# Kernel tuning notes

Measured on AMD Instinct MI355X. Metric: run time of the kernel, lower is better.

## Reference

```python
import jax, jax.numpy as jnp
import numpy as np

B, L, D, NUM_NODES = 256, 512, 128, 1024


def setup_inputs() -> dict:
    key = jax.random.key(0)
    k1, k2, k3, k4, k5, k6 = jax.random.split(key, 6)
    src_ids = jax.random.randint(k1, (B, L), 0, NUM_NODES, dtype=jnp.int32)
    dst_ids = jax.random.randint(k2, (B, L), 0, NUM_NODES, dtype=jnp.int32)
    s = 1.0  # nn.Linear default init is uniform; randn is fine for a numeric baseline
    W1 = jax.random.normal(k3, (1, D), dtype=jnp.float32) * s
    b1 = jax.random.normal(k4, (D,), dtype=jnp.float32) * 0.01
    W2 = jax.random.normal(k5, (D, D), dtype=jnp.float32) * (1.0 / np.sqrt(D))
    b2 = jax.random.normal(k6, (D,), dtype=jnp.float32) * 0.01
    return {"src_ids": src_ids, "dst_ids": dst_ids, "W1": W1, "b1": b1, "W2": W2, "b2": b2}


def _counts_in(a, b):
    # counts_in[i, j] = number of occurrences of a[i, j] within b[i, :]
    # matches np.unique counts / dict-lookup semantics (missing key -> 0)
    return (a[:, :, None] == b[:, None, :]).sum(axis=-1).astype(jnp.float32)


def _encode(appearances, W1, b1, W2, b2):
    # appearances: (B, L, 2) -> unsqueeze(-1) -> Linear(1, D) -> ReLU -> Linear(D, D) -> sum over the 2 count channels
    h = jax.nn.relu(appearances[..., None] * W1[0] + b1)      # (B, L, 2, D)
    h = jnp.einsum('blcd,de->blce', h, W2) + b2               # (B, L, 2, D)
    return h.sum(axis=2)                                      # (B, L, D)


def reference(src_ids, dst_ids, W1, b1, W2, b2):
    # co-occurrence appearance counts
    src_app = jnp.stack([_counts_in(src_ids, src_ids), _counts_in(src_ids, dst_ids)], axis=-1)  # (B, Ls, 2)
    dst_app = jnp.stack([_counts_in(dst_ids, src_ids), _counts_in(dst_ids, dst_ids)], axis=-1)  # (B, Ld, 2)
    # zero out padded positions (node id == 0)
    src_app = jnp.where(src_ids[..., None] == 0, 0.0, src_app)
    dst_app = jnp.where(dst_ids[..., None] == 0, 0.0, dst_app)
    src_feat = _encode(src_app, W1, b1, W2, b2)
    dst_feat = _encode(dst_app, W1, b1, W2, b2)
    return src_feat, dst_feat
```

## Files before the change

### kernel.cpp

```cpp
#include <hip/hip_runtime.h>


#define BB      256
#define LL      512
#define DD      128
#define NNODES  1024
#define SPLITS  4
#define ROWS_PER (LL / SPLITS)
#define CMAXP1  (LL + 1)
#define TBL_SLOTS 64

typedef float f4x __attribute__((ext_vector_type(4)));

__global__ __launch_bounds__(256) void fused_encode_kernel(
    const int* __restrict__ src_ids, const int* __restrict__ dst_ids,
    const float* __restrict__ W1, const float* __restrict__ b1,
    const float* __restrict__ W2, const float* __restrict__ b2,
    float* __restrict__ out) {
  __shared__ __align__(16) float tbl[TBL_SLOTS * DD];
  __shared__ int slotOf[CMAXP1];
  __shared__ int cnt[4 * ROWS_PER];
  __shared__ int cOf[TBL_SLOTS];
  __shared__ int ns;

  int* hist = (int*)tbl;

  const int batch = blockIdx.x >> 2;
  const int split = blockIdx.x & (SPLITS - 1);
  const int tid   = threadIdx.x;

#pragma unroll
  for (int i = tid; i < 2 * NNODES; i += 256) hist[i] = 0;
  for (int i = tid; i < CMAXP1; i += 256) slotOf[i] = -1;
  if (tid == 0) ns = 0;
  __syncthreads();

  const int* sb = src_ids + batch * LL;
  const int* db = dst_ids + batch * LL;
#pragma unroll
  for (int i = tid; i < LL; i += 256) {
    atomicAdd(&hist[sb[i]], 1);
    atomicAdd(&hist[NNODES + db[i]], 1);
  }
  __syncthreads();

  const int r0 = split * ROWS_PER;
#pragma unroll
  for (int i = tid; i < 4 * ROWS_PER; i += 256) {
    const int r  = i & (ROWS_PER - 1);
    const int g  = i >> 7;
    const int id = (g < 2 ? sb : db)[r0 + r];
    const int c  = id ? hist[(g & 1) * NNODES + id] : 0;
    cnt[i] = c;
    slotOf[c] = 1;
  }
  __syncthreads();

  for (int c = tid; c < CMAXP1; c += 256) {
    if (slotOf[c] >= 0) {
      const int s = atomicAdd(&ns, 1);
      slotOf[c] = s;
      cOf[s] = c;
    }
  }
  __syncthreads();

#pragma unroll
  for (int i = tid; i < 4 * ROWS_PER; i += 256) cnt[i] = slotOf[cnt[i]];

  {
    const int nslots = ns;
    const int e = tid & (DD - 1);
    for (int s = tid >> 7; s < nslots; s += 2) {
      const float fc = (float)cOf[s];
      float acc = b2[e];
#pragma unroll 16
      for (int d = 0; d < DD; ++d)
        acc = fmaf(fmaxf(fmaf(fc, W1[d], b1[d]), 0.0f), W2[d * DD + e], acc);
      tbl[s * DD + e] = acc;
    }
  }
  __syncthreads();

  const int lane = tid & 31;
  const int rsub = tid >> 5;
  float* out_s = out + ((size_t)batch * LL + r0) * DD;
  float* out_d = out_s + (size_t)BB * LL * DD;
  const f4x* tb = (const f4x*)tbl;

#pragma unroll 4
  for (int rr = rsub; rr < ROWS_PER; rr += 8) {
    const f4x a = tb[cnt[rr] * (DD / 4) + lane];
    const f4x b = tb[cnt[ROWS_PER + rr] * (DD / 4) + lane];
    const f4x c = tb[cnt[2 * ROWS_PER + rr] * (DD / 4) + lane];
    const f4x d = tb[cnt[3 * ROWS_PER + rr] * (DD / 4) + lane];
    __builtin_nontemporal_store(a + b, ((f4x*)(out_s + (size_t)rr * DD)) + lane);
    __builtin_nontemporal_store(c + d, ((f4x*)(out_d + (size_t)rr * DD)) + lane);
  }
}

extern "C" void kernel_launch(void* const* d_in, const int* in_sizes, int n_in,
                              void* d_out, int out_size, void* d_ws, size_t ws_size,
                              hipStream_t stream) {
  const int*   src = (const int*)d_in[0];
  const int*   dst = (const int*)d_in[1];
  const float* W1  = (const float*)d_in[2];
  const float* b1  = (const float*)d_in[3];
  const float* W2  = (const float*)d_in[4];
  const float* b2  = (const float*)d_in[5];
  fused_encode_kernel<<<BB * SPLITS, 256, 0, stream>>>(
      src, dst, W1, b1, W2, b2, (float*)d_out);
}
```

Before: 164.0 us.

## Use one 1024-thread block per batch with packed histogram and direct-indexed count table

Replaces four 256-thread blocks per batch with a single 1024-thread block, which removes the histogram work each split block used to redo. Src and dst counts are packed into one int histogram (low and high 16 bits), and a 32-bit mask records which counts below 32 appear. Encoded rows are precomputed only for those counts and indexed directly by count value, so the slot-remapping pass goes away. Counts of 32 or more fall back to a per-lane slow path that recomputes the row. That path is correct but costly, and it will almost never run for these random inputs.

```diff
diff --git a/kernel.cpp b/kernel.cpp
--- a/kernel.cpp
+++ b/kernel.cpp
@@ -5,97 +5,99 @@
 #define LL      512
 #define DD      128
 #define NNODES  1024
-#define SPLITS  4
-#define ROWS_PER (LL / SPLITS)
-#define CMAXP1  (LL + 1)
-#define TBL_SLOTS 64
+#define TBL_C   32
 
 typedef float f4x __attribute__((ext_vector_type(4)));
 
-__global__ __launch_bounds__(256) void fused_encode_kernel(
+__device__ __noinline__ f4x slow_row(int c, int lane,
+                                     const float* __restrict__ W1,
+                                     const float* __restrict__ b1,
+                                     const float* __restrict__ W2,
+                                     const float* __restrict__ b2) {
+  const int e0 = lane * 4;
+  f4x acc = { b2[e0], b2[e0 + 1], b2[e0 + 2], b2[e0 + 3] };
+  for (int d = 0; d < DD; ++d) {
+    const float h = fmaxf(fmaf((float)c, W1[d], b1[d]), 0.0f);
+#pragma unroll
+    for (int j = 0; j < 4; ++j) acc[j] = fmaf(h, W2[d * DD + e0 + j], acc[j]);
+  }
+  return acc;
+}
+
+__global__ __launch_bounds__(1024) void fused_encode_kernel(
     const int* __restrict__ src_ids, const int* __restrict__ dst_ids,
     const float* __restrict__ W1, const float* __restrict__ b1,
     const float* __restrict__ W2, const float* __restrict__ b2,
     float* __restrict__ out) {
-  __shared__ __align__(16) float tbl[TBL_SLOTS * DD];
-  __shared__ int slotOf[CMAXP1];
-  __shared__ int cnt[4 * ROWS_PER];
-  __shared__ int cOf[TBL_SLOTS];
-  __shared__ int ns;
+  __shared__ __align__(16) float tbl[TBL_C * DD];
+  __shared__ short cnt4[LL][4];
+  __shared__ int bitc[TBL_C];
+  __shared__ int nb, mask;
 
   int* hist = (int*)tbl;
 
-  const int batch = blockIdx.x >> 2;
-  const int split = blockIdx.x & (SPLITS - 1);
+  const int batch = blockIdx.x;
   const int tid   = threadIdx.x;
 
-#pragma unroll
-  for (int i = tid; i < 2 * NNODES; i += 256) hist[i] = 0;
-  for (int i = tid; i < CMAXP1; i += 256) slotOf[i] = -1;
-  if (tid == 0) ns = 0;
+  hist[tid] = 0;
+  if (tid == 0) { nb = 0; mask = 0; }
   __syncthreads();
 
   const int* sb = src_ids + batch * LL;
   const int* db = dst_ids + batch * LL;
+  if (tid < LL) atomicAdd(&hist[sb[tid]], 1);
+  else          atomicAdd(&hist[db[tid - LL]], 0x10000);
+  __syncthreads();
+
 #pragma unroll
-  for (int i = tid; i < LL; i += 256) {
-    atomicAdd(&hist[sb[i]], 1);
-    atomicAdd(&hist[NNODES + db[i]], 1);
+  for (int i = tid; i < 4 * LL; i += 1024) {
+    const int g  = i >> 9;
+    const int r  = i & (LL - 1);
+    const int id = (g < 2 ? sb : db)[r];
+    const int hv = id ? hist[id] : 0;
+    const int c  = (g & 1) ? (hv >> 16) : (hv & 0xffff);
+    cnt4[r][g] = (short)c;
+    if (c < TBL_C) atomicOr(&mask, 1u << c);
   }
   __syncthreads();
 
-  const int r0 = split * ROWS_PER;
-#pragma unroll
-  for (int i = tid; i < 4 * ROWS_PER; i += 256) {
-    const int r  = i & (ROWS_PER - 1);
-    const int g  = i >> 7;
-    const int id = (g < 2 ? sb : db)[r0 + r];
-    const int c  = id ? hist[(g & 1) * NNODES + id] : 0;
-    cnt[i] = c;
-    slotOf[c] = 1;
+  if (tid < TBL_C && ((mask >> tid) & 1)) {
+    const int p = atomicAdd(&nb, 1);
+    bitc[p] = tid;
   }
   __syncthreads();
 
-  for (int c = tid; c < CMAXP1; c += 256) {
-    if (slotOf[c] >= 0) {
-      const int s = atomicAdd(&ns, 1);
-      slotOf[c] = s;
-      cOf[s] = c;
-    }
-  }
-  __syncthreads();
-
-#pragma unroll
-  for (int i = tid; i < 4 * ROWS_PER; i += 256) cnt[i] = slotOf[cnt[i]];
-
   {
-    const int nslots = ns;
+    const int nrows = nb;
     const int e = tid & (DD - 1);
-    for (int s = tid >> 7; s < nslots; s += 2) {
-      const float fc = (float)cOf[s];
+    for (int k = tid >> 7; k < nrows; k += 8) {
+      const int   c  = bitc[k];
+      const float fc = (float)c;
       float acc = b2[e];
 #pragma unroll 16
       for (int d = 0; d < DD; ++d)
         acc = fmaf(fmaxf(fmaf(fc, W1[d], b1[d]), 0.0f), W2[d * DD + e], acc);
-      tbl[s * DD + e] = acc;
+      tbl[c * DD + e] = acc;
     }
   }
   __syncthreads();
 
   const int lane = tid & 31;
   const int rsub = tid >> 5;
-  float* out_s = out + ((size_t)batch * LL + r0) * DD;
+  float* out_s = out + (size_t)batch * LL * DD;
   float* out_d = out_s + (size_t)BB * LL * DD;
   const f4x* tb = (const f4x*)tbl;
 
 #pragma unroll 4
-  for (int rr = rsub; rr < ROWS_PER; rr += 8) {
-    const f4x a = tb[cnt[rr] * (DD / 4) + lane];
-    const f4x b = tb[cnt[ROWS_PER + rr] * (DD / 4) + lane];
-    const f4x c = tb[cnt[2 * ROWS_PER + rr] * (DD / 4) + lane];
-    const f4x d = tb[cnt[3 * ROWS_PER + rr] * (DD / 4) + lane];
-    __builtin_nontemporal_store(a + b, ((f4x*)(out_s + (size_t)rr * DD)) + lane);
-    __builtin_nontemporal_store(c + d, ((f4x*)(out_d + (size_t)rr * DD)) + lane);
+  for (int rr = rsub; rr < LL; rr += 32) {
+    const int ca = cnt4[rr][0], cb = cnt4[rr][1];
+    const int cc = cnt4[rr][2], cd = cnt4[rr][3];
+    const f4x va = (ca < TBL_C) ? tb[ca * (DD / 4) + lane] : slow_row(ca, lane, W1, b1, W2, b2);
+    const f4x vb = (cb < TBL_C) ? tb[cb * (DD / 4) + lane] : slow_row(cb, lane, W1, b1, W2, b2);
+    const f4x vc = (cc < TBL_C) ? tb[cc * (DD / 4) + lane] : slow_row(cc, lane, W1, b1, W2, b2);
+    const f4x vd = (cd < TBL_C) ? tb[cd * (DD / 4) + lane] : slow_row(cd, lane, W1, b1, W2, b2);
+    __builtin_nontemporal_store(va + vb, ((f4x*)(out_s + (size_t)rr * DD)) + lane);
+    __builtin_nontemporal_store(vc + vd, ((f4x*)(out_d + (size_t)rr * DD)) + lane);
   }
 }
 
@@ -108,6 +110,6 @@
   const float* b1  = (const float*)d_in[3];
   const float* W2  = (const float*)d_in[4];
   const float* b2  = (const float*)d_in[5];
-  fused_encode_kernel<<<BB * SPLITS, 256, 0, stream>>>(
-      src, dst, W1, b1, W2, b2, (float*)d_out);
+  fused_encode_kernel<<<BB, 1024, 0, stream>>>(src, dst, W1, b1, W2, b2,
+                                               (float*)d_out);
 }
```

Result: no change. 161.3 us (-1.7%).
